# Optimization experiments

Hardware: AMD Instinct MI355X
Metric: run time of the kernel (lower is better)

Reference implementation:

```python
import jax, jax.numpy as jnp
import numpy as np

N_NODES = 100000


def setup_inputs() -> dict:
    key = jax.random.key(0)
    k1, k2, k3 = jax.random.split(key, 3)
    x = jax.random.normal(k1, (N_NODES, 256), dtype=jnp.float32)
    edge_index = jax.random.randint(k2, (2, 1600000), 0, N_NODES, dtype=jnp.int64)
    # GCNConv learned params (glorot weight, zero bias as in PyG init)
    W = jax.random.normal(k3, (256, 64), dtype=jnp.float32) * (1.0 / np.sqrt(256.0))
    b = jnp.zeros((64,), dtype=jnp.float32)
    return {"x": x, "edge_index": edge_index, "W": W, "b": b}


def reference(x, edge_index, W, b):
    n = x.shape[0]
    # --- gcn_norm: add self-loops, symmetric normalization ---
    loops = jnp.arange(n, dtype=edge_index.dtype)
    row = jnp.concatenate([edge_index[0], loops])  # source nodes
    col = jnp.concatenate([edge_index[1], loops])  # target nodes
    ones = jnp.ones(row.shape[0], dtype=x.dtype)
    deg = jax.ops.segment_sum(ones, col, num_segments=n)  # [N]
    dinv = jnp.where(deg > 0, jax.lax.rsqrt(deg), 0.0)
    norm = dinv[row] * dinv[col]  # [E+N]
    # --- linear transform then normalized scatter-add aggregation ---
    h = x @ W  # [N, out]
    msgs = h[row] * norm[:, None]  # [E+N, out]
    out = jax.ops.segment_sum(msgs, col, num_segments=n)  # [N, out]
    return out + b
```

## Files before the change

kernel.cpp:

```cpp
#include <hip/hip_runtime.h>


#define IN_F 256
#define OUT_F 64
#define WBITS 8
#define MAXBINS 512
#define ROWMASK 0xFFFFFFu
#define SCAT_BLOCKS 512

typedef unsigned short ushort_t;
typedef short bf16x8 __attribute__((ext_vector_type(8)));
typedef float f32x4 __attribute__((ext_vector_type(4)));

static __device__ __forceinline__ unsigned f2bf1(float f) {
    unsigned u = __float_as_uint(f);
    return (u + 0x7FFFu + ((u >> 16) & 1u)) >> 16;
}
static __device__ __forceinline__ unsigned pk2(float a, float b) {
    return f2bf1(a) | (f2bf1(b) << 16);
}
static __device__ __forceinline__ ushort_t f2bf(float f) { return (ushort_t)f2bf1(f); }
static __device__ __forceinline__ float bf2f(ushort_t h) {
    return __uint_as_float(((unsigned)h) << 16);
}

__global__ __launch_bounds__(256) void init_kernel(const float* __restrict__ W,
                                                   ushort_t* __restrict__ wfrag,
                                                   const int* __restrict__ col,
                                                   int* __restrict__ binCnt,
                                                   int E, int nbins) {
    int gt = blockIdx.x * 256 + threadIdx.x;
    if (gt < 2048) {
        int t = gt;
        int kk = t >> 8;
        int ct = (t >> 6) & 3;
        int l  = t & 63;
        int k0 = kk * 32 + (l >> 4) * 8;
        int c  = ct * 16 + (l & 15);
        unsigned u0 = pk2(W[(k0 + 0) * OUT_F + c], W[(k0 + 1) * OUT_F + c]);
        unsigned u1 = pk2(W[(k0 + 2) * OUT_F + c], W[(k0 + 3) * OUT_F + c]);
        unsigned u2 = pk2(W[(k0 + 4) * OUT_F + c], W[(k0 + 5) * OUT_F + c]);
        unsigned u3 = pk2(W[(k0 + 6) * OUT_F + c], W[(k0 + 7) * OUT_F + c]);
        ((uint4*)wfrag)[t] = make_uint4(u0, u1, u2, u3);
    }
    __shared__ int hist[MAXBINS];
    int tid = threadIdx.x;
    for (int i = tid; i < nbins; i += 256) hist[i] = 0;
    __syncthreads();
    int stride = gridDim.x * 256;
    for (int e = blockIdx.x * 256 + tid; e < E; e += stride)
        atomicAdd(&hist[col[e] >> WBITS], 1);
    __syncthreads();
    for (int i = tid; i < nbins; i += 256)
        if (hist[i]) atomicAdd(&binCnt[i], hist[i]);
}

__global__ void bin_scan_kernel(const int* __restrict__ binCnt, int* __restrict__ binStart,
                                int* __restrict__ binCursor, int* __restrict__ start_n,
                                int nbins) {
    __shared__ int lds[512];
    int tid = threadIdx.x;
    int v = (tid < nbins) ? binCnt[tid] : 0;
    lds[tid] = v;
    __syncthreads();
    for (int d = 1; d < 512; d <<= 1) {
        int t = (tid >= d) ? lds[tid - d] : 0;
        __syncthreads();
        lds[tid] += t;
        __syncthreads();
    }
    if (tid < nbins) {
        int ex = lds[tid] - v;
        binStart[tid] = ex;
        binCursor[tid] = ex;
    }
    if (tid == 511) {
        binStart[nbins] = lds[511];
        start_n[0] = lds[511];
    }
}

__global__ __launch_bounds__(256) void mega_kernel(const float* __restrict__ x,
                                                   const ushort_t* __restrict__ wfrag,
                                                   ushort_t* __restrict__ h,
                                                   const int* __restrict__ row,
                                                   const int* __restrict__ col,
                                                   int* __restrict__ binCursor,
                                                   unsigned* __restrict__ ebuf,
                                                   int n, int E, int nbins, int gemmBlocks) {
    __shared__ int cnt[MAXBINS];
    __shared__ int cur[MAXBINS];
    int tid = threadIdx.x;

    if (blockIdx.x < gemmBlocks) {
        int l  = tid & 63;
        int lr = l & 15;
        int lg = l >> 4;
        int rowbase = blockIdx.x * 64 + (tid >> 6) * 16;
        int arow = rowbase + lr;
        int lrow = (arow < n) ? arow : (n - 1);
        const float* xp = x + (size_t)lrow * IN_F + lg * 8;
        const uint4* wf = (const uint4*)wfrag;

        f32x4 acc0 = {0.f, 0.f, 0.f, 0.f};
        f32x4 acc1 = {0.f, 0.f, 0.f, 0.f};
        f32x4 acc2 = {0.f, 0.f, 0.f, 0.f};
        f32x4 acc3 = {0.f, 0.f, 0.f, 0.f};

        #pragma unroll
        for (int kk = 0; kk < 8; ++kk) {
            float4 xa = *(const float4*)(xp + kk * 32);
            float4 xb = *(const float4*)(xp + kk * 32 + 4);
            union { bf16x8 v; unsigned u[4]; } A;
            A.u[0] = pk2(xa.x, xa.y);
            A.u[1] = pk2(xa.z, xa.w);
            A.u[2] = pk2(xb.x, xb.y);
            A.u[3] = pk2(xb.z, xb.w);
            union { uint4 q; bf16x8 v; } B0, B1, B2, B3;
            B0.q = wf[(kk * 4 + 0) * 64 + l];
            B1.q = wf[(kk * 4 + 1) * 64 + l];
            B2.q = wf[(kk * 4 + 2) * 64 + l];
            B3.q = wf[(kk * 4 + 3) * 64 + l];
            acc0 = __builtin_amdgcn_mfma_f32_16x16x32_bf16(A.v, B0.v, acc0, 0, 0, 0);
            acc1 = __builtin_amdgcn_mfma_f32_16x16x32_bf16(A.v, B1.v, acc1, 0, 0, 0);
            acc2 = __builtin_amdgcn_mfma_f32_16x16x32_bf16(A.v, B2.v, acc2, 0, 0, 0);
            acc3 = __builtin_amdgcn_mfma_f32_16x16x32_bf16(A.v, B3.v, acc3, 0, 0, 0);
        }

        #pragma unroll
        for (int q = 0; q < 4; ++q) {
            int r = rowbase + lg * 4 + q;
            if (r < n) {
                ushort_t* gp = h + (size_t)r * OUT_F + lr;
                gp[0]  = f2bf(acc0[q]);
                gp[16] = f2bf(acc1[q]);
                gp[32] = f2bf(acc2[q]);
                gp[48] = f2bf(acc3[q]);
            }
        }
    } else {
        int sb = blockIdx.x - gemmBlocks;
        for (int i = tid; i < nbins; i += 256) cnt[i] = 0;
        __syncthreads();
        int chunk = (E + SCAT_BLOCKS - 1) / SCAT_BLOCKS;
        int s = sb * chunk;
        int epos = min(E, s + chunk);
        for (int e = s + tid; e < epos; e += 256)
            atomicAdd(&cnt[col[e] >> WBITS], 1);
        __syncthreads();
        for (int i = tid; i < nbins; i += 256) {
            int c = cnt[i];
            cur[i] = c ? atomicAdd(&binCursor[i], c) : 0;
        }
        __syncthreads();
        for (int e = s + tid; e < epos; e += 256) {
            int cc = col[e];
            int pos = atomicAdd(&cur[cc >> WBITS], 1);
            ebuf[pos] = (unsigned)row[e] | ((unsigned)(cc & ((1 << WBITS) - 1)) << 24);
        }
    }
}

__global__ __launch_bounds__(256) void fine_build_kernel(const unsigned* __restrict__ ebuf,
                                                         const int* __restrict__ binStart,
                                                         int* __restrict__ start,
                                                         float* __restrict__ dinv,
                                                         int* __restrict__ bucket,
                                                         ushort_t* __restrict__ g, int n) {
    __shared__ int sdeg[256];
    __shared__ int scur[256];
    __shared__ float sdv[256];
    int b = blockIdx.x;
    int lo = b << WBITS;
    int wcnt = min(256, n - lo);
    int tid = threadIdx.x;
    sdeg[tid] = 0;
    __syncthreads();
    int s = binStart[b], epos = binStart[b + 1];
    for (int e = s + tid; e < epos; e += 256)
        atomicAdd(&sdeg[ebuf[e] >> 24], 1);
    __syncthreads();
    int d = sdeg[tid];
    float dv = rsqrtf((float)(d + 1));
    sdv[tid] = dv;
    if (tid < wcnt) dinv[lo + tid] = dv;
    for (int dd = 1; dd < 256; dd <<= 1) {
        int t = (tid >= dd) ? sdeg[tid - dd] : 0;
        __syncthreads();
        sdeg[tid] += t;
        __syncthreads();
    }
    int ex = sdeg[tid] - d;
    if (tid < wcnt) start[lo + tid] = s + ex;
    scur[tid] = ex;
    __syncthreads();
    for (int e = s + tid; e < epos; e += 256) {
        unsigned pr = ebuf[e];
        int pos = atomicAdd(&scur[pr >> 24], 1);
        bucket[s + pos] = (int)(pr & ROWMASK);
    }
    unsigned* gw = (unsigned*)(g + (size_t)lo * OUT_F);
    int total = wcnt * 32;
    for (int idx = tid; idx < total; idx += 256) {
        unsigned u = gw[idx];
        float sc = sdv[idx >> 5];
        float a = bf2f((ushort_t)(u & 0xFFFF)) * sc;
        float c = bf2f((ushort_t)(u >> 16)) * sc;
        gw[idx] = pk2(a, c);
    }
}

__global__ __launch_bounds__(256) void gather_kernel(const int* __restrict__ start,
                              const int* __restrict__ bucket, const ushort_t* __restrict__ g,
                              const float* __restrict__ dinv, const float* __restrict__ b,
                              float* __restrict__ out, int n) {
    int lane = threadIdx.x & 63;
    int node = blockIdx.x * 4 + (threadIdx.x >> 6);
    if (node >= n) return;
    int f4  = lane & 15;
    int grp = lane >> 4;
    int s0  = start[node];
    int cnt = start[node + 1] - s0;
    const int* bp = bucket + s0;
    int last = cnt - 1;

    float4 aA = {0,0,0,0}, aB = {0,0,0,0}, aC = {0,0,0,0}, aD = {0,0,0,0};
    for (int e0 = 0; e0 < cnt; e0 += 16) {
        int eA = e0 + grp;
        int eB = e0 + 4 + grp;
        int eC = e0 + 8 + grp;
        int eD = e0 + 12 + grp;
        int iA = bp[min(eA, last)];
        int iB = bp[min(eB, last)];
        int iC = bp[min(eC, last)];
        int iD = bp[min(eD, last)];
        ushort4 vA = *(const ushort4*)(g + (size_t)iA * OUT_F + f4 * 4);
        ushort4 vB = *(const ushort4*)(g + (size_t)iB * OUT_F + f4 * 4);
        ushort4 vC = *(const ushort4*)(g + (size_t)iC * OUT_F + f4 * 4);
        ushort4 vD = *(const ushort4*)(g + (size_t)iD * OUT_F + f4 * 4);
        aA.x += (eA < cnt) ? bf2f(vA.x) : 0.f;
        aA.y += (eA < cnt) ? bf2f(vA.y) : 0.f;
        aA.z += (eA < cnt) ? bf2f(vA.z) : 0.f;
        aA.w += (eA < cnt) ? bf2f(vA.w) : 0.f;
        aB.x += (eB < cnt) ? bf2f(vB.x) : 0.f;
        aB.y += (eB < cnt) ? bf2f(vB.y) : 0.f;
        aB.z += (eB < cnt) ? bf2f(vB.z) : 0.f;
        aB.w += (eB < cnt) ? bf2f(vB.w) : 0.f;
        aC.x += (eC < cnt) ? bf2f(vC.x) : 0.f;
        aC.y += (eC < cnt) ? bf2f(vC.y) : 0.f;
        aC.z += (eC < cnt) ? bf2f(vC.z) : 0.f;
        aC.w += (eC < cnt) ? bf2f(vC.w) : 0.f;
        aD.x += (eD < cnt) ? bf2f(vD.x) : 0.f;
        aD.y += (eD < cnt) ? bf2f(vD.y) : 0.f;
        aD.z += (eD < cnt) ? bf2f(vD.z) : 0.f;
        aD.w += (eD < cnt) ? bf2f(vD.w) : 0.f;
    }
    float4 acc;
    acc.x = (aA.x + aB.x) + (aC.x + aD.x);
    acc.y = (aA.y + aB.y) + (aC.y + aD.y);
    acc.z = (aA.z + aB.z) + (aC.z + aD.z);
    acc.w = (aA.w + aB.w) + (aC.w + aD.w);
    acc.x += __shfl_xor(acc.x, 16, 64);
    acc.y += __shfl_xor(acc.y, 16, 64);
    acc.z += __shfl_xor(acc.z, 16, 64);
    acc.w += __shfl_xor(acc.w, 16, 64);
    acc.x += __shfl_xor(acc.x, 32, 64);
    acc.y += __shfl_xor(acc.y, 32, 64);
    acc.z += __shfl_xor(acc.z, 32, 64);
    acc.w += __shfl_xor(acc.w, 32, 64);

    if (grp == 0) {
        ushort4 sv = *(const ushort4*)(g + (size_t)node * OUT_F + f4 * 4);
        float dc = dinv[node];
        float4 bv = ((const float4*)b)[f4];
        float4 o;
        o.x = (acc.x + bf2f(sv.x)) * dc + bv.x;
        o.y = (acc.y + bf2f(sv.y)) * dc + bv.y;
        o.z = (acc.z + bf2f(sv.z)) * dc + bv.z;
        o.w = (acc.w + bf2f(sv.w)) * dc + bv.w;
        ((float4*)(out + (size_t)node * OUT_F))[f4] = o;
    }
}

extern "C" void kernel_launch(void* const* d_in, const int* in_sizes, int n_in,
                              void* d_out, int out_size, void* d_ws, size_t ws_size,
                              hipStream_t stream) {
    const float* x  = (const float*)d_in[0];
    const int*   ei = (const int*)d_in[1];
    const float* W  = (const float*)d_in[2];
    const float* b  = (const float*)d_in[3];
    float* out = (float*)d_out;

    int n = in_sizes[0] / IN_F;
    int E = in_sizes[1] / 2;
    const int* rowp = ei;
    const int* colp = ei + E;

    int nbins = (n + 255) >> WBITS;

    char* wp = (char*)d_ws;
    ushort_t* g    = (ushort_t*)wp;
    unsigned* ebuf = (unsigned*)(wp + (size_t)n * OUT_F * 2);
    int* bucket    = (int*)(ebuf + E);
    ushort_t* wfrag = (ushort_t*)(bucket + E);
    int* start     = (int*)(wfrag + 16384);
    float* dinv    = (float*)(start + n + 1);
    int* binCnt    = (int*)(dinv + n);
    int* binStart  = binCnt + MAXBINS;
    int* binCursor = binStart + MAXBINS + 1;

    int gemmBlocks = (n + 63) / 64;

    hipMemsetAsync(binCnt, 0, MAXBINS * sizeof(int), stream);
    init_kernel<<<512, 256, 0, stream>>>(W, wfrag, colp, binCnt, E, nbins);
    bin_scan_kernel<<<1, 512, 0, stream>>>(binCnt, binStart, binCursor, start + n, nbins);
    mega_kernel<<<gemmBlocks + SCAT_BLOCKS, 256, 0, stream>>>(x, wfrag, g, rowp, colp,
                                                              binCursor, ebuf, n, E, nbins,
                                                              gemmBlocks);
    fine_build_kernel<<<nbins, 256, 0, stream>>>(ebuf, binStart, start, dinv, bucket, g, n);
    gather_kernel<<<(n + 3) / 4, 256, 0, stream>>>(start, bucket, g, dinv, b, out, n);
}
```

Measured before the change: 151.6 us.

## Schedule scatter blocks first with fewer blocks; widen gather loads to 16 bytes

The fused GEMM/scatter kernel now places the edge-binning blocks at the front of the grid and cuts their count from 512 to 128. The long-running scatter work is dispatched first and overlaps with the GEMM blocks instead of trailing behind them, with fewer global cursor atomics. The gather kernel now has each lane load 8 bf16 values (uint4) per neighbor with 8 neighbor groups, instead of 4 values with 16 groups. This halves the number of load instructions per edge. The cost is larger per-block scatter chunks and more accumulator registers in the gather.

```diff
diff --git a/kernel.cpp b/kernel.cpp
--- a/kernel.cpp
+++ b/kernel.cpp
@@ -6,7 +6,7 @@
 #define WBITS 8
 #define MAXBINS 512
 #define ROWMASK 0xFFFFFFu
-#define SCAT_BLOCKS 512
+#define SCAT_BLOCKS 128
 
 typedef unsigned short ushort_t;
 typedef short bf16x8 __attribute__((ext_vector_type(8)));
@@ -87,16 +87,37 @@
                                                    const int* __restrict__ col,
                                                    int* __restrict__ binCursor,
                                                    unsigned* __restrict__ ebuf,
-                                                   int n, int E, int nbins, int gemmBlocks) {
+                                                   int n, int E, int nbins) {
     __shared__ int cnt[MAXBINS];
     __shared__ int cur[MAXBINS];
     int tid = threadIdx.x;
 
-    if (blockIdx.x < gemmBlocks) {
+    if (blockIdx.x < SCAT_BLOCKS) {
+        int sb = blockIdx.x;
+        for (int i = tid; i < nbins; i += 256) cnt[i] = 0;
+        __syncthreads();
+        int chunk = (E + SCAT_BLOCKS - 1) / SCAT_BLOCKS;
+        int s = sb * chunk;
+        int epos = min(E, s + chunk);
+        for (int e = s + tid; e < epos; e += 256)
+            atomicAdd(&cnt[col[e] >> WBITS], 1);
+        __syncthreads();
+        for (int i = tid; i < nbins; i += 256) {
+            int c = cnt[i];
+            cur[i] = c ? atomicAdd(&binCursor[i], c) : 0;
+        }
+        __syncthreads();
+        for (int e = s + tid; e < epos; e += 256) {
+            int cc = col[e];
+            int pos = atomicAdd(&cur[cc >> WBITS], 1);
+            ebuf[pos] = (unsigned)row[e] | ((unsigned)(cc & ((1 << WBITS) - 1)) << 24);
+        }
+    } else {
+        int gb = blockIdx.x - SCAT_BLOCKS;
         int l  = tid & 63;
         int lr = l & 15;
         int lg = l >> 4;
-        int rowbase = blockIdx.x * 64 + (tid >> 6) * 16;
+        int rowbase = gb * 64 + (tid >> 6) * 16;
         int arow = rowbase + lr;
         int lrow = (arow < n) ? arow : (n - 1);
         const float* xp = x + (size_t)lrow * IN_F + lg * 8;
@@ -138,26 +159,6 @@
                 gp[48] = f2bf(acc3[q]);
             }
         }
-    } else {
-        int sb = blockIdx.x - gemmBlocks;
-        for (int i = tid; i < nbins; i += 256) cnt[i] = 0;
-        __syncthreads();
-        int chunk = (E + SCAT_BLOCKS - 1) / SCAT_BLOCKS;
-        int s = sb * chunk;
-        int epos = min(E, s + chunk);
-        for (int e = s + tid; e < epos; e += 256)
-            atomicAdd(&cnt[col[e] >> WBITS], 1);
-        __syncthreads();
-        for (int i = tid; i < nbins; i += 256) {
-            int c = cnt[i];
-            cur[i] = c ? atomicAdd(&binCursor[i], c) : 0;
-        }
-        __syncthreads();
-        for (int e = s + tid; e < epos; e += 256) {
-            int cc = col[e];
-            int pos = atomicAdd(&cur[cc >> WBITS], 1);
-            ebuf[pos] = (unsigned)row[e] | ((unsigned)(cc & ((1 << WBITS) - 1)) << 24);
-        }
     }
 }
 
@@ -217,68 +218,70 @@
     int lane = threadIdx.x & 63;
     int node = blockIdx.x * 4 + (threadIdx.x >> 6);
     if (node >= n) return;
-    int f4  = lane & 15;
-    int grp = lane >> 4;
+    int f8  = lane & 7;
+    int grp = lane >> 3;
     int s0  = start[node];
     int cnt = start[node + 1] - s0;
     const int* bp = bucket + s0;
     int last = cnt - 1;
 
-    float4 aA = {0,0,0,0}, aB = {0,0,0,0}, aC = {0,0,0,0}, aD = {0,0,0,0};
+    float a0 = 0.f, a1 = 0.f, a2 = 0.f, a3 = 0.f;
+    float a4 = 0.f, a5 = 0.f, a6 = 0.f, a7 = 0.f;
+    union { uint4 q; ushort_t s[8]; } VA, VB;
     for (int e0 = 0; e0 < cnt; e0 += 16) {
         int eA = e0 + grp;
-        int eB = e0 + 4 + grp;
-        int eC = e0 + 8 + grp;
-        int eD = e0 + 12 + grp;
+        int eB = e0 + 8 + grp;
         int iA = bp[min(eA, last)];
         int iB = bp[min(eB, last)];
-        int iC = bp[min(eC, last)];
-        int iD = bp[min(eD, last)];
-        ushort4 vA = *(const ushort4*)(g + (size_t)iA * OUT_F + f4 * 4);
-        ushort4 vB = *(const ushort4*)(g + (size_t)iB * OUT_F + f4 * 4);
-        ushort4 vC = *(const ushort4*)(g + (size_t)iC * OUT_F + f4 * 4);
-        ushort4 vD = *(const ushort4*)(g + (size_t)iD * OUT_F + f4 * 4);
-        aA.x += (eA < cnt) ? bf2f(vA.x) : 0.f;
-        aA.y += (eA < cnt) ? bf2f(vA.y) : 0.f;
-        aA.z += (eA < cnt) ? bf2f(vA.z) : 0.f;
-        aA.w += (eA < cnt) ? bf2f(vA.w) : 0.f;
-        aB.x += (eB < cnt) ? bf2f(vB.x) : 0.f;
-        aB.y += (eB < cnt) ? bf2f(vB.y) : 0.f;
-        aB.z += (eB < cnt) ? bf2f(vB.z) : 0.f;
-        aB.w += (eB < cnt) ? bf2f(vB.w) : 0.f;
-        aC.x += (eC < cnt) ? bf2f(vC.x) : 0.f;
-        aC.y += (eC < cnt) ? bf2f(vC.y) : 0.f;
-        aC.z += (eC < cnt) ? bf2f(vC.z) : 0.f;
-        aC.w += (eC < cnt) ? bf2f(vC.w) : 0.f;
-        aD.x += (eD < cnt) ? bf2f(vD.x) : 0.f;
-        aD.y += (eD < cnt) ? bf2f(vD.y) : 0.f;
-        aD.z += (eD < cnt) ? bf2f(vD.z) : 0.f;
-        aD.w += (eD < cnt) ? bf2f(vD.w) : 0.f;
-    }
-    float4 acc;
-    acc.x = (aA.x + aB.x) + (aC.x + aD.x);
-    acc.y = (aA.y + aB.y) + (aC.y + aD.y);
-    acc.z = (aA.z + aB.z) + (aC.z + aD.z);
-    acc.w = (aA.w + aB.w) + (aC.w + aD.w);
-    acc.x += __shfl_xor(acc.x, 16, 64);
-    acc.y += __shfl_xor(acc.y, 16, 64);
-    acc.z += __shfl_xor(acc.z, 16, 64);
-    acc.w += __shfl_xor(acc.w, 16, 64);
-    acc.x += __shfl_xor(acc.x, 32, 64);
-    acc.y += __shfl_xor(acc.y, 32, 64);
-    acc.z += __shfl_xor(acc.z, 32, 64);
-    acc.w += __shfl_xor(acc.w, 32, 64);
+        VA.q = *(const uint4*)(g + (size_t)iA * OUT_F + f8 * 8);
+        VB.q = *(const uint4*)(g + (size_t)iB * OUT_F + f8 * 8);
+        bool mA = eA < cnt, mB = eB < cnt;
+        a0 += mA ? bf2f(VA.s[0]) : 0.f;
+        a1 += mA ? bf2f(VA.s[1]) : 0.f;
+        a2 += mA ? bf2f(VA.s[2]) : 0.f;
+        a3 += mA ? bf2f(VA.s[3]) : 0.f;
+        a4 += mA ? bf2f(VA.s[4]) : 0.f;
+        a5 += mA ? bf2f(VA.s[5]) : 0.f;
+        a6 += mA ? bf2f(VA.s[6]) : 0.f;
+        a7 += mA ? bf2f(VA.s[7]) : 0.f;
+        a0 += mB ? bf2f(VB.s[0]) : 0.f;
+        a1 += mB ? bf2f(VB.s[1]) : 0.f;
+        a2 += mB ? bf2f(VB.s[2]) : 0.f;
+        a3 += mB ? bf2f(VB.s[3]) : 0.f;
+        a4 += mB ? bf2f(VB.s[4]) : 0.f;
+        a5 += mB ? bf2f(VB.s[5]) : 0.f;
+        a6 += mB ? bf2f(VB.s[6]) : 0.f;
+        a7 += mB ? bf2f(VB.s[7]) : 0.f;
+    }
+    #pragma unroll
+    for (int off = 8; off < 64; off <<= 1) {
+        a0 += __shfl_xor(a0, off, 64);
+        a1 += __shfl_xor(a1, off, 64);
+        a2 += __shfl_xor(a2, off, 64);
+        a3 += __shfl_xor(a3, off, 64);
+        a4 += __shfl_xor(a4, off, 64);
+        a5 += __shfl_xor(a5, off, 64);
+        a6 += __shfl_xor(a6, off, 64);
+        a7 += __shfl_xor(a7, off, 64);
+    }
 
     if (grp == 0) {
-        ushort4 sv = *(const ushort4*)(g + (size_t)node * OUT_F + f4 * 4);
+        union { uint4 q; ushort_t s[8]; } SV;
+        SV.q = *(const uint4*)(g + (size_t)node * OUT_F + f8 * 8);
         float dc = dinv[node];
-        float4 bv = ((const float4*)b)[f4];
-        float4 o;
-        o.x = (acc.x + bf2f(sv.x)) * dc + bv.x;
-        o.y = (acc.y + bf2f(sv.y)) * dc + bv.y;
-        o.z = (acc.z + bf2f(sv.z)) * dc + bv.z;
-        o.w = (acc.w + bf2f(sv.w)) * dc + bv.w;
-        ((float4*)(out + (size_t)node * OUT_F))[f4] = o;
+        const float4* bv = (const float4*)b;
+        float4 o0, o1;
+        o0.x = (a0 + bf2f(SV.s[0])) * dc + bv[f8 * 2].x;
+        o0.y = (a1 + bf2f(SV.s[1])) * dc + bv[f8 * 2].y;
+        o0.z = (a2 + bf2f(SV.s[2])) * dc + bv[f8 * 2].z;
+        o0.w = (a3 + bf2f(SV.s[3])) * dc + bv[f8 * 2].w;
+        o1.x = (a4 + bf2f(SV.s[4])) * dc + bv[f8 * 2 + 1].x;
+        o1.y = (a5 + bf2f(SV.s[5])) * dc + bv[f8 * 2 + 1].y;
+        o1.z = (a6 + bf2f(SV.s[6])) * dc + bv[f8 * 2 + 1].z;
+        o1.w = (a7 + bf2f(SV.s[7])) * dc + bv[f8 * 2 + 1].w;
+        float4* op = (float4*)(out + (size_t)node * OUT_F + f8 * 8);
+        op[0] = o0;
+        op[1] = o1;
     }
 }
 
@@ -314,9 +317,8 @@
     hipMemsetAsync(binCnt, 0, MAXBINS * sizeof(int), stream);
     init_kernel<<<512, 256, 0, stream>>>(W, wfrag, colp, binCnt, E, nbins);
     bin_scan_kernel<<<1, 512, 0, stream>>>(binCnt, binStart, binCursor, start + n, nbins);
-    mega_kernel<<<gemmBlocks + SCAT_BLOCKS, 256, 0, stream>>>(x, wfrag, g, rowp, colp,
-                                                              binCursor, ebuf, n, E, nbins,
-                                                              gemmBlocks);
+    mega_kernel<<<SCAT_BLOCKS + gemmBlocks, 256, 0, stream>>>(x, wfrag, g, rowp, colp,
+                                                              binCursor, ebuf, n, E, nbins);
     fine_build_kernel<<<nbins, 256, 0, stream>>>(ebuf, binStart, start, dinv, bucket, g, n);
     gather_kernel<<<(n + 3) / 4, 256, 0, stream>>>(start, bucket, g, dinv, b, out, n);
 }
```

After: 164.6 us. +8.5%, slower.
